# Optimization experiments

Hardware: AMD Instinct MI355X
Metric: run time of the kernel (lower is better)

## Reference

```python
import jax, jax.numpy as jnp
import numpy as np

# --- static config (matches init_kwargs) ---
N = 10000          # nodes
E = 160000         # edges
MULT = 16          # multiplicity (in and out)
NL = 2             # number of irreps (lvals = [0, 1])
DIM = 4            # 1 + 3 spherical dims
EDGE_DIM = 32
HID = 128
RANK = 8           # low-rank radial weight rank
H = 4              # attention heads
HM = MULT // H     # head multiplicity
IDX = np.array([0, 1, 1, 1])  # irrep index for each of the DIM positions


def _radial(ef, w1, bb1, wl, bl, wr, br):
    """Low-rank radial weight: (E, edge_dim) -> (E, NL*MULT, NL*MULT)."""
    h = jax.nn.gelu(ef @ w1 + bb1, approximate=False)
    left = (h @ wl + bl).reshape(-1, NL * MULT, RANK)
    right = (h @ wr + br).reshape(-1, RANK, NL * MULT)
    return left @ right


def _conv(b1, b2, ef, f, src, w1, bb1, wl, bl, wr, br):
    """Equivariant convolution: gather -> basis contract -> radial bmm -> basis."""
    rw = _radial(ef, w1, bb1, wl, bl, wr, br)          # (E, 2*MULT, 2*MULT)
    f_src = f[src]                                      # (E, MULT, DIM)
    t = jnp.einsum('emd,edl->eml', f_src, b1)           # (E, MULT, NL)
    t = t.reshape(E, MULT * NL)                         # row-major, matches torch view
    t = jnp.einsum('erc,ec->er', rw, t)                 # (E, NL*MULT)
    t = t.reshape(E, MULT, NL)                          # (E, out_mult, nl2)
    return jnp.einsum('eml,eld->emd', t, b2)            # (E, MULT, DIM)


def reference(b1, b2, edge_feats, f, src_idx, dst_idx,
              q_w, q_b,
              k_w1, k_b1, k_wl, k_bl, k_wr, k_br,
              v_w1, v_b1, v_wl, v_bl, v_wr, v_br):
    # --- Q: equivariant linear on node features (per-irrep weights) ---
    W = q_w.reshape(NL, MULT, MULT)[IDX]                # (DIM, out_mult, in_mult)
    q = jnp.einsum('dom,nmd->nod', W, f)                # (N, MULT, DIM)
    q = q.at[:, :, 0].add(q_b[:, 0])                    # bias on scalar (l=0) slot

    # --- K, V: equivariant convolutions over edges ---
    k = _conv(b1, b2, edge_feats, f, src_idx, k_w1, k_b1, k_wl, k_bl, k_wr, k_br)
    v = _conv(b1, b2, edge_feats, f, src_idx, v_w1, v_b1, v_wl, v_bl, v_wr, v_br)

    # --- multi-head node_wise attention scores ---
    qh = q.reshape(N, H, HM * DIM)
    kh = k.reshape(E, H, HM * DIM)
    scale = jnp.sqrt(jnp.asarray(HM * DIM, q.dtype))
    scores = jnp.sum(qh[dst_idx] * kh, axis=-1) / scale  # (E, H)

    # --- segment softmax over edges grouped by destination node ---
    m = jax.ops.segment_max(scores, dst_idx, num_segments=N)       # (N, H)
    ex = jnp.exp(scores - m[dst_idx])
    den = jax.ops.segment_sum(ex, dst_idx, num_segments=N)         # (N, H)
    alpha = ex / jnp.maximum(den[dst_idx], 1e-9)                   # (E, H)

    # --- weighted scatter-reduce of values ---
    vh = v.reshape(E, H, HM * DIM)
    out = jax.ops.segment_sum(alpha[..., None] * vh, dst_idx, num_segments=N)
    return out.reshape(N, MULT, DIM)


def setup_inputs() -> dict:
    key = jax.random.key(0)
    ks = jax.random.split(key, 24)
    s = 0.05
    inp = {
        'b1': jax.random.normal(ks[0], (E, DIM, NL), jnp.float32),
        'b2': jax.random.normal(ks[1], (E, NL, DIM), jnp.float32),
        'edge_feats': jax.random.normal(ks[2], (E, EDGE_DIM), jnp.float32),
        'f': jax.random.normal(ks[3], (N, MULT, DIM), jnp.float32),
        'src_idx': jax.random.randint(ks[4], (E,), 0, N),
        'dst_idx': jax.random.randint(ks[5], (E,), 0, N),
        # Q equivariant linear
        'q_w': jax.random.normal(ks[6], (NL * MULT, MULT), jnp.float32) * s,
        'q_b': jnp.zeros((MULT, 1), jnp.float32),
    }
    for i, p in enumerate(['k', 'v']):
        base = 8 + i * 6
        inp[p + '_w1'] = jax.random.normal(ks[base + 0], (EDGE_DIM, HID), jnp.float32) * s
        inp[p + '_b1'] = jnp.zeros((HID,), jnp.float32)
        inp[p + '_wl'] = jax.random.normal(ks[base + 2], (HID, NL * MULT * RANK), jnp.float32) * s
        inp[p + '_bl'] = jnp.zeros((NL * MULT * RANK,), jnp.float32)
        inp[p + '_wr'] = jax.random.normal(ks[base + 4], (HID, RANK * NL * MULT), jnp.float32) * s
        inp[p + '_br'] = jnp.zeros((RANK * NL * MULT,), jnp.float32)
    return inp
```

## Files before the change

kernel.cpp:

```cpp
#include <hip/hip_runtime.h>
#include <hip/hip_bf16.h>
#include <math.h>

#define NNODES 10000
#define NEDGE  160000

typedef unsigned short u16;
using bf16x8 = __attribute__((ext_vector_type(8))) short;
using u16x8  = __attribute__((ext_vector_type(8))) unsigned short;
using f32x4  = __attribute__((ext_vector_type(4))) float;

static __device__ __forceinline__ u16 f2bf(float x) {
  unsigned u = __float_as_uint(x);
  u += 0x7FFFu + ((u >> 16) & 1u);
  return (u16)(u >> 16);
}
static __device__ __forceinline__ float bf2f(u16 h) {
  return __uint_as_float(((unsigned)h) << 16);
}
static __device__ __forceinline__ float fast_gelu(float x) {
  float y = x * __builtin_fmaf(0.07135481283f, x * x, 1.5957691216f);
  float e = __expf(y);
  return x - x * __builtin_amdgcn_rcpf(e + 1.0f);
}

__global__ void __launch_bounds__(256) setup_kernel(
    const float* __restrict__ kwr, const float* __restrict__ kwl,
    const float* __restrict__ vwr, const float* __restrict__ vwl,
    u16* __restrict__ Wsw,
    const float* __restrict__ kw1, const float* __restrict__ vw1,
    u16* __restrict__ W1sw,
    const float* __restrict__ f, const float* __restrict__ qw,
    const float* __restrict__ qb, float* __restrict__ q,
    int* __restrict__ cnt) {
  int b = blockIdx.x, tid = threadIdx.x;
  if (b < 40) {
    int i = b * 256 + tid;
    if (i < NNODES) cnt[i] = 0;
  } else if (b < 552) {
    int idx = (b - 40) * 256 + tid;
    int slot = idx >> 15;
    int w = idx & 32767;
    int j = w & 7, lane = (w >> 3) & 63, ks = (w >> 9) & 3, tg = w >> 11;
    int k   = ks * 32 + ((lane >> 4) << 3) + j;
    int col = (tg << 4) + (lane & 15);
    const float* s = (slot == 0) ? kwr : (slot == 1) ? kwl : (slot == 2) ? vwr : vwl;
    Wsw[idx] = f2bf(s[k * 256 + col]);
  } else if (b < 584) {
    int idx = (b - 552) * 256 + tid;
    int slot = idx >> 12;
    int w = idx & 4095;
    int j = w & 7, lane = (w >> 3) & 63, nt = w >> 9;
    int k   = ((lane >> 4) << 3) + j;
    int col = (nt << 4) + (lane & 15);
    const float* s = (slot == 0) ? kw1 : vw1;
    W1sw[idx] = f2bf(s[k * 128 + col]);
  } else {
    int i = (b - 584) * 256 + tid;
    if (i >= NNODES * 16) return;
    int n = i >> 4, o = i & 15;
    const float* frow = f + (size_t)n * 64;
    float o0 = 0.f, o1 = 0.f, o2 = 0.f, o3 = 0.f;
#pragma unroll
    for (int m = 0; m < 16; ++m) {
      float w0 = qw[o * 16 + m];
      float w1 = qw[(16 + o) * 16 + m];
      o0 += w0 * frow[m * 4 + 0];
      o1 += w1 * frow[m * 4 + 1];
      o2 += w1 * frow[m * 4 + 2];
      o3 += w1 * frow[m * 4 + 3];
    }
    o0 += qb[o];
    float4 r = make_float4(o0, o1, o2, o3);
    *(float4*)(q + (size_t)i * 4) = r;
  }
}

__global__ void csr_count_kernel(const int* __restrict__ dst, int* __restrict__ cnt) {
  int e = blockIdx.x * 256 + threadIdx.x;
  atomicAdd(&cnt[dst[e]], 1);
}
__global__ void __launch_bounds__(1024) csr_scan_kernel(
    const int* __restrict__ cnt, int* __restrict__ rowptr, int* __restrict__ cursor) {
  __shared__ int part[1024];
  int t = threadIdx.x;
  int base = t * 10;
  int s = 0;
#pragma unroll
  for (int i = 0; i < 10; ++i) { int idx = base + i; if (idx < NNODES) s += cnt[idx]; }
  part[t] = s;
  __syncthreads();
  for (int o = 1; o < 1024; o <<= 1) {
    int v = (t >= o) ? part[t - o] : 0;
    __syncthreads();
    part[t] += v;
    __syncthreads();
  }
  int run = (t == 0) ? 0 : part[t - 1];
#pragma unroll
  for (int i = 0; i < 10; ++i) {
    int idx = base + i;
    if (idx < NNODES) { rowptr[idx] = run; cursor[idx] = run; run += cnt[idx]; }
  }
  if (t == 1023) rowptr[NNODES] = run;
}
__global__ void csr_fill_kernel(const int* __restrict__ dst, int* __restrict__ cursor,
                                int* __restrict__ eidx) {
  int e = blockIdx.x * 256 + threadIdx.x;
  int pos = atomicAdd(&cursor[dst[e]], 1);
  eidx[pos] = e;
}

__global__ void t_kernel(const float* __restrict__ f, const float* __restrict__ b1,
                         const int* __restrict__ src, const int* __restrict__ eidx,
                         const float* __restrict__ b2,
                         u16* __restrict__ tbuf, float* __restrict__ b2p) {
  int i = blockIdx.x * 256 + threadIdx.x;
  int re = eidx[i];
  const float* frow = f + (size_t)src[re] * 64;
  const float* be = b1 + (size_t)re * 8;
  float b[8];
#pragma unroll
  for (int k = 0; k < 8; ++k) b[k] = be[k];
  u16* tp = tbuf + (size_t)i * 32;
#pragma unroll
  for (int mh = 0; mh < 4; ++mh) {
    u16x8 ov;
#pragma unroll
    for (int mi = 0; mi < 4; ++mi) {
      int m = mh * 4 + mi;
      float f0 = frow[m * 4 + 0], f1 = frow[m * 4 + 1], f2 = frow[m * 4 + 2], f3 = frow[m * 4 + 3];
#pragma unroll
      for (int l = 0; l < 2; ++l) {
        float t = f0 * b[0 * 2 + l] + f1 * b[1 * 2 + l] + f2 * b[2 * 2 + l] + f3 * b[3 * 2 + l];
        ov[mi * 2 + l] = f2bf(t);
      }
    }
    *(u16x8*)&tp[mh * 8] = ov;
  }
  const float* b2e = b2 + (size_t)re * 8;
  float* bp = b2p + (size_t)i * 8;
  *(float4*)&bp[0] = *(const float4*)&b2e[0];
  *(float4*)&bp[4] = *(const float4*)&b2e[4];
}

__global__ void __launch_bounds__(512) conv_fused_kernel(
    const float* __restrict__ ef, const u16* __restrict__ w1sw,
    const float* __restrict__ b1h,
    const u16* __restrict__ wsw_r, const float* __restrict__ br,
    const u16* __restrict__ wsw_l, const float* __restrict__ bl,
    const u16* __restrict__ tbuf, const float* __restrict__ b2p,
    const int* __restrict__ eidx, u16* __restrict__ kv) {
  __shared__ alignas(16) u16 sA[64 * 136];
  __shared__ alignas(16) u16 t_s[64 * 40];
  __shared__ alignas(16) float b2_s[64 * 12];
  __shared__ alignas(16) float u_s[64 * 12];
  __shared__ alignas(16) float t2_pool[64 * 36];
  float* t2_s = t2_pool;
  u16*   efs  = (u16*)t2_pool;

  int tid = threadIdx.x;
  int wave = tid >> 6, lane = tid & 63, quad = lane >> 4, l16 = lane & 15;
  size_t i0 = (size_t)blockIdx.x * 64;

  if (tid < 256) {
    int row = tid >> 2, seg = tid & 3;
    int pe = eidx[i0 + row];
    const float* ap = ef + (size_t)pe * 32 + seg * 8;
    float4 v0 = *(const float4*)&ap[0];
    float4 v1 = *(const float4*)&ap[4];
    u16x8 ov;
    ov[0] = f2bf(v0.x); ov[1] = f2bf(v0.y); ov[2] = f2bf(v0.z); ov[3] = f2bf(v0.w);
    ov[4] = f2bf(v1.x); ov[5] = f2bf(v1.y); ov[6] = f2bf(v1.z); ov[7] = f2bf(v1.w);
    *(u16x8*)&efs[row * 40 + seg * 8] = ov;
    if (tid < 128) {
      int r2 = tid >> 1, half = tid & 1;
      *(float4*)&b2_s[r2 * 12 + half * 4] = *(const float4*)&b2p[(i0 + r2) * 8 + half * 4];
    }
  } else {
    int j = tid - 256;
    int row = j >> 2, seg = j & 3;
    *(uint4*)&t_s[row * 40 + seg * 8] = *(const uint4*)&tbuf[(i0 + row) * 32 + seg * 8];
  }
  __syncthreads();

  {
    bf16x8 aw = *(const bf16x8*)&w1sw[(size_t)(wave * 64 + lane) * 8];
    float4 bias_h = *(const float4*)&b1h[wave * 16 + quad * 4];
#pragma unroll
    for (int nt = 0; nt < 4; ++nt) {
      bf16x8 be = *(const bf16x8*)&efs[(nt * 16 + l16) * 40 + quad * 8];
      f32x4 acch = __builtin_amdgcn_mfma_f32_16x16x32_bf16(aw, be, (f32x4){0.f, 0.f, 0.f, 0.f}, 0, 0, 0);
      ushort4 hv;
      hv.x = f2bf(fast_gelu(acch[0] + bias_h.x));
      hv.y = f2bf(fast_gelu(acch[1] + bias_h.y));
      hv.z = f2bf(fast_gelu(acch[2] + bias_h.z));
      hv.w = f2bf(fast_gelu(acch[3] + bias_h.w));
      *(ushort4*)&sA[(nt * 16 + l16) * 136 + wave * 16 + quad * 4] = hv;
    }
  }
  __syncthreads();

  f32x4 accr[2][4], accl[2][4];
#pragma unroll
  for (int mtl = 0; mtl < 2; ++mtl)
#pragma unroll
    for (int nt = 0; nt < 4; ++nt) {
      accr[mtl][nt] = (f32x4){0.f, 0.f, 0.f, 0.f};
      accl[mtl][nt] = (f32x4){0.f, 0.f, 0.f, 0.f};
    }
#pragma unroll
  for (int ks = 0; ks < 4; ++ks) {
    bf16x8 bfrag[4];
#pragma unroll
    for (int nt = 0; nt < 4; ++nt)
      bfrag[nt] = *(const bf16x8*)&sA[(nt * 16 + l16) * 136 + ks * 32 + quad * 8];
#pragma unroll
    for (int mtl = 0; mtl < 2; ++mtl) {
      int mtg = wave * 2 + mtl;
      bf16x8 ar = *(const bf16x8*)&wsw_r[(size_t)((mtg * 4 + ks) * 64 + lane) * 8];
      bf16x8 al = *(const bf16x8*)&wsw_l[(size_t)((mtg * 4 + ks) * 64 + lane) * 8];
#pragma unroll
      for (int nt = 0; nt < 4; ++nt) {
        accr[mtl][nt] = __builtin_amdgcn_mfma_f32_16x16x32_bf16(ar, bfrag[nt], accr[mtl][nt], 0, 0, 0);
        accl[mtl][nt] = __builtin_amdgcn_mfma_f32_16x16x32_bf16(al, bfrag[nt], accl[mtl][nt], 0, 0, 0);
      }
    }
  }

  float brv[2][4], blv[2][4];
#pragma unroll
  for (int mtl = 0; mtl < 2; ++mtl)
#pragma unroll
    for (int r = 0; r < 4; ++r) {
      int col = (wave * 2 + mtl) * 16 + quad * 4 + r;
      brv[mtl][r] = br[col];
      blv[mtl][r] = bl[col];
    }

#pragma unroll
  for (int nt = 0; nt < 4; ++nt) {
    int e = nt * 16 + l16;
    ushort4 ta = *(const ushort4*)&t_s[e * 40 + 4 * quad];
    ushort4 tb = *(const ushort4*)&t_s[e * 40 + 16 + 4 * quad];
    float s = (accr[0][nt][0] + brv[0][0]) * bf2f(ta.x)
            + (accr[0][nt][1] + brv[0][1]) * bf2f(ta.y)
            + (accr[0][nt][2] + brv[0][2]) * bf2f(ta.z)
            + (accr[0][nt][3] + brv[0][3]) * bf2f(ta.w)
            + (accr[1][nt][0] + brv[1][0]) * bf2f(tb.x)
            + (accr[1][nt][1] + brv[1][1]) * bf2f(tb.y)
            + (accr[1][nt][2] + brv[1][2]) * bf2f(tb.z)
            + (accr[1][nt][3] + brv[1][3]) * bf2f(tb.w);
    s += __shfl_xor(s, 16);
    s += __shfl_xor(s, 32);
    if (quad == 0) u_s[e * 12 + wave] = s;
  }
  __syncthreads();

#pragma unroll
  for (int nt = 0; nt < 4; ++nt) {
    int e = nt * 16 + l16;
    float4 uv = *(const float4*)&u_s[e * 12 + 4 * (quad & 1)];
#pragma unroll
    for (int mtl = 0; mtl < 2; ++mtl) {
      float s = (accl[mtl][nt][0] + blv[mtl][0]) * uv.x
              + (accl[mtl][nt][1] + blv[mtl][1]) * uv.y
              + (accl[mtl][nt][2] + blv[mtl][2]) * uv.z
              + (accl[mtl][nt][3] + blv[mtl][3]) * uv.w;
      s += __shfl_xor(s, 16);
      if ((quad & 1) == 0)
        t2_s[e * 36 + 4 * wave + 2 * mtl + (quad >> 1)] = s;
    }
  }
  __syncthreads();

  {
    int e = tid >> 3, j = tid & 7;
    float4 t2 = *(const float4*)&t2_s[e * 36 + 4 * j];
    float4 b2a = *(const float4*)&b2_s[e * 12 + 0];
    float4 b2b = *(const float4*)&b2_s[e * 12 + 4];
    u16x8 ov;
    ov[0] = f2bf(t2.x * b2a.x + t2.y * b2b.x);
    ov[1] = f2bf(t2.x * b2a.y + t2.y * b2b.y);
    ov[2] = f2bf(t2.x * b2a.z + t2.y * b2b.z);
    ov[3] = f2bf(t2.x * b2a.w + t2.y * b2b.w);
    ov[4] = f2bf(t2.z * b2a.x + t2.w * b2b.x);
    ov[5] = f2bf(t2.z * b2a.y + t2.w * b2b.y);
    ov[6] = f2bf(t2.z * b2a.z + t2.w * b2b.z);
    ov[7] = f2bf(t2.z * b2a.w + t2.w * b2b.w);
    *(u16x8*)&kv[(i0 + e) * 64 + j * 8] = ov;
  }
}

__global__ void __launch_bounds__(256) attn_gather_kernel(
    const float* __restrict__ q, const u16* __restrict__ kvk,
    const u16* __restrict__ kvv, const int* __restrict__ rowptr,
    float* __restrict__ outp) {
  int tid = threadIdx.x;
  int node = blockIdx.x * 4 + (tid >> 6);
  int lane = tid & 63;
  float qv = q[(size_t)node * 64 + lane];
  int beg = rowptr[node], end = rowptr[node + 1];
  float num = 0.f, den = 0.f;
  for (int idx = beg; idx < end; ++idx) {
    float kf = bf2f(kvk[(size_t)idx * 64 + lane]);
    float p = qv * kf;
    p += __shfl_xor(p, 1, 16);
    p += __shfl_xor(p, 2, 16);
    p += __shfl_xor(p, 4, 16);
    p += __shfl_xor(p, 8, 16);
    float exv = __expf(p * 0.25f);
    den += exv;
    num += exv * bf2f(kvv[(size_t)idx * 64 + lane]);
  }
  outp[(size_t)node * 64 + lane] = num / fmaxf(den, 1e-9f);
}

extern "C" void kernel_launch(void* const* d_in, const int* in_sizes, int n_in,
                              void* d_out, int out_size, void* d_ws, size_t ws_size,
                              hipStream_t stream) {
  const float* b1  = (const float*)d_in[0];
  const float* b2  = (const float*)d_in[1];
  const float* ef  = (const float*)d_in[2];
  const float* f   = (const float*)d_in[3];
  const int*   src = (const int*)d_in[4];
  const int*   dst = (const int*)d_in[5];
  const float* qw  = (const float*)d_in[6];
  const float* qb  = (const float*)d_in[7];
  const float* kw1 = (const float*)d_in[8];
  const float* kb1 = (const float*)d_in[9];
  const float* kwl = (const float*)d_in[10];
  const float* kbl = (const float*)d_in[11];
  const float* kwr = (const float*)d_in[12];
  const float* kbr = (const float*)d_in[13];
  const float* vw1 = (const float*)d_in[14];
  const float* vb1 = (const float*)d_in[15];
  const float* vwl = (const float*)d_in[16];
  const float* vbl = (const float*)d_in[17];
  const float* vwr = (const float*)d_in[18];
  const float* vbr = (const float*)d_in[19];
  float* outp = (float*)d_out;

  char* ws = (char*)d_ws;
  size_t off = 0;
  auto alloc = [&](size_t bytes) {
    char* p = ws + off;
    off += (bytes + 511) & ~(size_t)511;
    return p;
  };
  u16*   Wsw  = (u16*)  alloc((size_t)4 * 32768 * 2);
  u16*   W1sw = (u16*)  alloc((size_t)2 * 4096 * 2);
  u16*   tbuf = (u16*)  alloc((size_t)NEDGE * 32 * 2);
  float* b2p  = (float*)alloc((size_t)NEDGE * 8 * 4);
  u16*   kvk  = (u16*)  alloc((size_t)NEDGE * 64 * 2);
  u16*   kvv  = (u16*)  alloc((size_t)NEDGE * 64 * 2);
  float* qbuf = (float*)alloc((size_t)NNODES * 64 * 4);
  int*   cnt    = (int*)alloc((size_t)NNODES * 4);
  int*   rowptr = (int*)alloc((size_t)(NNODES + 1) * 4);
  int*   cursor = (int*)alloc((size_t)NNODES * 4);
  int*   eidx   = (int*)alloc((size_t)NEDGE * 4);

  setup_kernel<<<1209, 256, 0, stream>>>(kwr, kwl, vwr, vwl, Wsw,
                                         kw1, vw1, W1sw,
                                         f, qw, qb, qbuf, cnt);
  csr_count_kernel<<<625, 256, 0, stream>>>(dst, cnt);
  csr_scan_kernel<<<1, 1024, 0, stream>>>(cnt, rowptr, cursor);
  csr_fill_kernel<<<625, 256, 0, stream>>>(dst, cursor, eidx);

  t_kernel<<<625, 256, 0, stream>>>(f, b1, src, eidx, b2, tbuf, b2p);

  conv_fused_kernel<<<2500, 512, 0, stream>>>(ef, W1sw + 0 * 4096, kb1,
                                              Wsw + 0 * 32768, kbr,
                                              Wsw + 1 * 32768, kbl,
                                              tbuf, b2p, eidx, kvk);
  conv_fused_kernel<<<2500, 512, 0, stream>>>(ef, W1sw + 1 * 4096, vb1,
                                              Wsw + 2 * 32768, vbr,
                                              Wsw + 3 * 32768, vbl,
                                              tbuf, b2p, eidx, kvv);

  attn_gather_kernel<<<2500, 256, 0, stream>>>(qbuf, kvk, kvv, rowptr, outp);
}
```

Measured before the change: 263.6 us.

## Fuse CSR fill with edge prep, pre-permute bf16 edge feats, seed MFMA with bias

Merges the CSR scatter and the per-edge t/b2 preparation into one kernel that writes directly at the sorted position. It also pre-converts edge features to bf16 in sorted order, so the conv kernels read them contiguously without an eidx indirection or an extra barrier. Biases are folded into the MFMA accumulator initial values, and bf16 packing uses paired conversions. The t2 stride changes to 33, and the attention reduction uses DPP instead of shuffles. The cost is an extra bf16 edge-feature buffer and scattered writes in the fill kernel.

```diff
diff --git a/kernel.cpp b/kernel.cpp
--- a/kernel.cpp
+++ b/kernel.cpp
@@ -18,10 +18,21 @@
 static __device__ __forceinline__ float bf2f(u16 h) {
   return __uint_as_float(((unsigned)h) << 16);
 }
+static __device__ __forceinline__ unsigned pack_bf16(float a, float b) {
+  __hip_bfloat162 h = __float22bfloat162_rn(make_float2(a, b));
+  return *(unsigned*)&h;
+}
 static __device__ __forceinline__ float fast_gelu(float x) {
   float y = x * __builtin_fmaf(0.07135481283f, x * x, 1.5957691216f);
   float e = __expf(y);
   return x - x * __builtin_amdgcn_rcpf(e + 1.0f);
+}
+static __device__ __forceinline__ float dpp_red16(float p) {
+  p += __int_as_float(__builtin_amdgcn_update_dpp(0, __float_as_int(p), 0xB1,  0xF, 0xF, true));
+  p += __int_as_float(__builtin_amdgcn_update_dpp(0, __float_as_int(p), 0x4E,  0xF, 0xF, true));
+  p += __int_as_float(__builtin_amdgcn_update_dpp(0, __float_as_int(p), 0x141, 0xF, 0xF, true));
+  p += __int_as_float(__builtin_amdgcn_update_dpp(0, __float_as_int(p), 0x140, 0xF, 0xF, true));
+  return p;
 }
 
 __global__ void __launch_bounds__(256) setup_kernel(
@@ -104,60 +115,61 @@
   }
   if (t == 1023) rowptr[NNODES] = run;
 }
-__global__ void csr_fill_kernel(const int* __restrict__ dst, int* __restrict__ cursor,
-                                int* __restrict__ eidx) {
+
+__global__ void __launch_bounds__(256) fill_t_kernel(
+    const int* __restrict__ dst, const int* __restrict__ src,
+    const float* __restrict__ f, const float* __restrict__ b1,
+    const float* __restrict__ b2, const float* __restrict__ ef,
+    int* __restrict__ cursor,
+    u16* __restrict__ tbuf, float* __restrict__ b2p, u16* __restrict__ efp) {
   int e = blockIdx.x * 256 + threadIdx.x;
   int pos = atomicAdd(&cursor[dst[e]], 1);
-  eidx[pos] = e;
-}
-
-__global__ void t_kernel(const float* __restrict__ f, const float* __restrict__ b1,
-                         const int* __restrict__ src, const int* __restrict__ eidx,
-                         const float* __restrict__ b2,
-                         u16* __restrict__ tbuf, float* __restrict__ b2p) {
-  int i = blockIdx.x * 256 + threadIdx.x;
-  int re = eidx[i];
-  const float* frow = f + (size_t)src[re] * 64;
-  const float* be = b1 + (size_t)re * 8;
+  const float* frow = f + (size_t)src[e] * 64;
+  const float* be = b1 + (size_t)e * 8;
   float b[8];
 #pragma unroll
   for (int k = 0; k < 8; ++k) b[k] = be[k];
-  u16* tp = tbuf + (size_t)i * 32;
+  uint4* tp = (uint4*)(tbuf + (size_t)pos * 32);
 #pragma unroll
   for (int mh = 0; mh < 4; ++mh) {
-    u16x8 ov;
+    unsigned pk[4];
 #pragma unroll
     for (int mi = 0; mi < 4; ++mi) {
       int m = mh * 4 + mi;
       float f0 = frow[m * 4 + 0], f1 = frow[m * 4 + 1], f2 = frow[m * 4 + 2], f3 = frow[m * 4 + 3];
-#pragma unroll
-      for (int l = 0; l < 2; ++l) {
-        float t = f0 * b[0 * 2 + l] + f1 * b[1 * 2 + l] + f2 * b[2 * 2 + l] + f3 * b[3 * 2 + l];
-        ov[mi * 2 + l] = f2bf(t);
-      }
-    }
-    *(u16x8*)&tp[mh * 8] = ov;
-  }
-  const float* b2e = b2 + (size_t)re * 8;
-  float* bp = b2p + (size_t)i * 8;
+      float t0 = f0 * b[0] + f1 * b[2] + f2 * b[4] + f3 * b[6];
+      float t1 = f0 * b[1] + f1 * b[3] + f2 * b[5] + f3 * b[7];
+      pk[mi] = pack_bf16(t0, t1);
+    }
+    tp[mh] = make_uint4(pk[0], pk[1], pk[2], pk[3]);
+  }
+  const float* b2e = b2 + (size_t)e * 8;
+  float* bp = b2p + (size_t)pos * 8;
   *(float4*)&bp[0] = *(const float4*)&b2e[0];
   *(float4*)&bp[4] = *(const float4*)&b2e[4];
+  const float* efe = ef + (size_t)e * 32;
+  uint4* ep = (uint4*)(efp + (size_t)pos * 32);
+#pragma unroll
+  for (int g = 0; g < 4; ++g) {
+    float4 v0 = *(const float4*)&efe[g * 8];
+    float4 v1 = *(const float4*)&efe[g * 8 + 4];
+    ep[g] = make_uint4(pack_bf16(v0.x, v0.y), pack_bf16(v0.z, v0.w),
+                       pack_bf16(v1.x, v1.y), pack_bf16(v1.z, v1.w));
+  }
 }
 
 __global__ void __launch_bounds__(512) conv_fused_kernel(
-    const float* __restrict__ ef, const u16* __restrict__ w1sw,
+    const u16* __restrict__ efp, const u16* __restrict__ w1sw,
     const float* __restrict__ b1h,
     const u16* __restrict__ wsw_r, const float* __restrict__ br,
     const u16* __restrict__ wsw_l, const float* __restrict__ bl,
     const u16* __restrict__ tbuf, const float* __restrict__ b2p,
-    const int* __restrict__ eidx, u16* __restrict__ kv) {
+    u16* __restrict__ kv) {
   __shared__ alignas(16) u16 sA[64 * 136];
   __shared__ alignas(16) u16 t_s[64 * 40];
   __shared__ alignas(16) float b2_s[64 * 12];
   __shared__ alignas(16) float u_s[64 * 12];
-  __shared__ alignas(16) float t2_pool[64 * 36];
-  float* t2_s = t2_pool;
-  u16*   efs  = (u16*)t2_pool;
+  __shared__ alignas(16) float t2_s[64 * 33];
 
   int tid = threadIdx.x;
   int wave = tid >> 6, lane = tid & 63, quad = lane >> 4, l16 = lane & 15;
@@ -165,50 +177,46 @@
 
   if (tid < 256) {
     int row = tid >> 2, seg = tid & 3;
-    int pe = eidx[i0 + row];
-    const float* ap = ef + (size_t)pe * 32 + seg * 8;
-    float4 v0 = *(const float4*)&ap[0];
-    float4 v1 = *(const float4*)&ap[4];
-    u16x8 ov;
-    ov[0] = f2bf(v0.x); ov[1] = f2bf(v0.y); ov[2] = f2bf(v0.z); ov[3] = f2bf(v0.w);
-    ov[4] = f2bf(v1.x); ov[5] = f2bf(v1.y); ov[6] = f2bf(v1.z); ov[7] = f2bf(v1.w);
-    *(u16x8*)&efs[row * 40 + seg * 8] = ov;
-    if (tid < 128) {
-      int r2 = tid >> 1, half = tid & 1;
-      *(float4*)&b2_s[r2 * 12 + half * 4] = *(const float4*)&b2p[(i0 + r2) * 8 + half * 4];
-    }
-  } else {
-    int j = tid - 256;
-    int row = j >> 2, seg = j & 3;
     *(uint4*)&t_s[row * 40 + seg * 8] = *(const uint4*)&tbuf[(i0 + row) * 32 + seg * 8];
-  }
-  __syncthreads();
+  } else if (tid < 384) {
+    int j = tid - 256, row = j >> 1, half = j & 1;
+    *(float4*)&b2_s[row * 12 + half * 4] = *(const float4*)&b2p[(i0 + row) * 8 + half * 4];
+  }
 
   {
     bf16x8 aw = *(const bf16x8*)&w1sw[(size_t)(wave * 64 + lane) * 8];
     float4 bias_h = *(const float4*)&b1h[wave * 16 + quad * 4];
+    f32x4 seed;
+    seed[0] = bias_h.x; seed[1] = bias_h.y; seed[2] = bias_h.z; seed[3] = bias_h.w;
 #pragma unroll
     for (int nt = 0; nt < 4; ++nt) {
-      bf16x8 be = *(const bf16x8*)&efs[(nt * 16 + l16) * 40 + quad * 8];
-      f32x4 acch = __builtin_amdgcn_mfma_f32_16x16x32_bf16(aw, be, (f32x4){0.f, 0.f, 0.f, 0.f}, 0, 0, 0);
-      ushort4 hv;
-      hv.x = f2bf(fast_gelu(acch[0] + bias_h.x));
-      hv.y = f2bf(fast_gelu(acch[1] + bias_h.y));
-      hv.z = f2bf(fast_gelu(acch[2] + bias_h.z));
-      hv.w = f2bf(fast_gelu(acch[3] + bias_h.w));
-      *(ushort4*)&sA[(nt * 16 + l16) * 136 + wave * 16 + quad * 4] = hv;
+      bf16x8 be = *(const bf16x8*)&efp[(i0 + nt * 16 + l16) * 32 + quad * 8];
+      f32x4 acch = __builtin_amdgcn_mfma_f32_16x16x32_bf16(aw, be, seed, 0, 0, 0);
+      unsigned p0 = pack_bf16(fast_gelu(acch[0]), fast_gelu(acch[1]));
+      unsigned p1 = pack_bf16(fast_gelu(acch[2]), fast_gelu(acch[3]));
+      *(uint2*)&sA[(nt * 16 + l16) * 136 + wave * 16 + quad * 4] = make_uint2(p0, p1);
     }
   }
   __syncthreads();
 
+  float4 brv[2], blv[2];
+#pragma unroll
+  for (int mtl = 0; mtl < 2; ++mtl) {
+    int colb = (wave * 2 + mtl) * 16 + quad * 4;
+    brv[mtl] = *(const float4*)&br[colb];
+    blv[mtl] = *(const float4*)&bl[colb];
+  }
   f32x4 accr[2][4], accl[2][4];
 #pragma unroll
   for (int mtl = 0; mtl < 2; ++mtl)
 #pragma unroll
     for (int nt = 0; nt < 4; ++nt) {
-      accr[mtl][nt] = (f32x4){0.f, 0.f, 0.f, 0.f};
-      accl[mtl][nt] = (f32x4){0.f, 0.f, 0.f, 0.f};
-    }
+      accr[mtl][nt][0] = brv[mtl].x; accr[mtl][nt][1] = brv[mtl].y;
+      accr[mtl][nt][2] = brv[mtl].z; accr[mtl][nt][3] = brv[mtl].w;
+      accl[mtl][nt][0] = blv[mtl].x; accl[mtl][nt][1] = blv[mtl].y;
+      accl[mtl][nt][2] = blv[mtl].z; accl[mtl][nt][3] = blv[mtl].w;
+    }
+
 #pragma unroll
   for (int ks = 0; ks < 4; ++ks) {
     bf16x8 bfrag[4];
@@ -228,29 +236,19 @@
     }
   }
 
-  float brv[2][4], blv[2][4];
-#pragma unroll
-  for (int mtl = 0; mtl < 2; ++mtl)
-#pragma unroll
-    for (int r = 0; r < 4; ++r) {
-      int col = (wave * 2 + mtl) * 16 + quad * 4 + r;
-      brv[mtl][r] = br[col];
-      blv[mtl][r] = bl[col];
-    }
-
 #pragma unroll
   for (int nt = 0; nt < 4; ++nt) {
     int e = nt * 16 + l16;
     ushort4 ta = *(const ushort4*)&t_s[e * 40 + 4 * quad];
     ushort4 tb = *(const ushort4*)&t_s[e * 40 + 16 + 4 * quad];
-    float s = (accr[0][nt][0] + brv[0][0]) * bf2f(ta.x)
-            + (accr[0][nt][1] + brv[0][1]) * bf2f(ta.y)
-            + (accr[0][nt][2] + brv[0][2]) * bf2f(ta.z)
-            + (accr[0][nt][3] + brv[0][3]) * bf2f(ta.w)
-            + (accr[1][nt][0] + brv[1][0]) * bf2f(tb.x)
-            + (accr[1][nt][1] + brv[1][1]) * bf2f(tb.y)
-            + (accr[1][nt][2] + brv[1][2]) * bf2f(tb.z)
-            + (accr[1][nt][3] + brv[1][3]) * bf2f(tb.w);
+    float s = accr[0][nt][0] * bf2f(ta.x)
+            + accr[0][nt][1] * bf2f(ta.y)
+            + accr[0][nt][2] * bf2f(ta.z)
+            + accr[0][nt][3] * bf2f(ta.w)
+            + accr[1][nt][0] * bf2f(tb.x)
+            + accr[1][nt][1] * bf2f(tb.y)
+            + accr[1][nt][2] * bf2f(tb.z)
+            + accr[1][nt][3] * bf2f(tb.w);
     s += __shfl_xor(s, 16);
     s += __shfl_xor(s, 32);
     if (quad == 0) u_s[e * 12 + wave] = s;
@@ -263,32 +261,28 @@
     float4 uv = *(const float4*)&u_s[e * 12 + 4 * (quad & 1)];
 #pragma unroll
     for (int mtl = 0; mtl < 2; ++mtl) {
-      float s = (accl[mtl][nt][0] + blv[mtl][0]) * uv.x
-              + (accl[mtl][nt][1] + blv[mtl][1]) * uv.y
-              + (accl[mtl][nt][2] + blv[mtl][2]) * uv.z
-              + (accl[mtl][nt][3] + blv[mtl][3]) * uv.w;
+      float s = accl[mtl][nt][0] * uv.x
+              + accl[mtl][nt][1] * uv.y
+              + accl[mtl][nt][2] * uv.z
+              + accl[mtl][nt][3] * uv.w;
       s += __shfl_xor(s, 16);
       if ((quad & 1) == 0)
-        t2_s[e * 36 + 4 * wave + 2 * mtl + (quad >> 1)] = s;
+        t2_s[e * 33 + 4 * wave + 2 * mtl + (quad >> 1)] = s;
     }
   }
   __syncthreads();
 
   {
     int e = tid >> 3, j = tid & 7;
-    float4 t2 = *(const float4*)&t2_s[e * 36 + 4 * j];
+    const float* tp = &t2_s[e * 33 + 4 * j];
+    float t20 = tp[0], t21 = tp[1], t22 = tp[2], t23 = tp[3];
     float4 b2a = *(const float4*)&b2_s[e * 12 + 0];
     float4 b2b = *(const float4*)&b2_s[e * 12 + 4];
-    u16x8 ov;
-    ov[0] = f2bf(t2.x * b2a.x + t2.y * b2b.x);
-    ov[1] = f2bf(t2.x * b2a.y + t2.y * b2b.y);
-    ov[2] = f2bf(t2.x * b2a.z + t2.y * b2b.z);
-    ov[3] = f2bf(t2.x * b2a.w + t2.y * b2b.w);
-    ov[4] = f2bf(t2.z * b2a.x + t2.w * b2b.x);
-    ov[5] = f2bf(t2.z * b2a.y + t2.w * b2b.y);
-    ov[6] = f2bf(t2.z * b2a.z + t2.w * b2b.z);
-    ov[7] = f2bf(t2.z * b2a.w + t2.w * b2b.w);
-    *(u16x8*)&kv[(i0 + e) * 64 + j * 8] = ov;
+    unsigned q0 = pack_bf16(t20 * b2a.x + t21 * b2b.x, t20 * b2a.y + t21 * b2b.y);
+    unsigned q1 = pack_bf16(t20 * b2a.z + t21 * b2b.z, t20 * b2a.w + t21 * b2b.w);
+    unsigned q2 = pack_bf16(t22 * b2a.x + t23 * b2b.x, t22 * b2a.y + t23 * b2b.y);
+    unsigned q3 = pack_bf16(t22 * b2a.z + t23 * b2b.z, t22 * b2a.w + t23 * b2b.w);
+    *(uint4*)&kv[(i0 + e) * 64 + j * 8] = make_uint4(q0, q1, q2, q3);
   }
 }
 
@@ -304,11 +298,7 @@
   float num = 0.f, den = 0.f;
   for (int idx = beg; idx < end; ++idx) {
     float kf = bf2f(kvk[(size_t)idx * 64 + lane]);
-    float p = qv * kf;
-    p += __shfl_xor(p, 1, 16);
-    p += __shfl_xor(p, 2, 16);
-    p += __shfl_xor(p, 4, 16);
-    p += __shfl_xor(p, 8, 16);
+    float p = dpp_red16(qv * kf);
     float exv = __expf(p * 0.25f);
     den += exv;
     num += exv * bf2f(kvv[(size_t)idx * 64 + lane]);
@@ -352,31 +342,30 @@
   u16*   W1sw = (u16*)  alloc((size_t)2 * 4096 * 2);
   u16*   tbuf = (u16*)  alloc((size_t)NEDGE * 32 * 2);
   float* b2p  = (float*)alloc((size_t)NEDGE * 8 * 4);
+  u16*   efp  = (u16*)  alloc((size_t)NEDGE * 32 * 2);
   u16*   kvk  = (u16*)  alloc((size_t)NEDGE * 64 * 2);
   u16*   kvv  = (u16*)  alloc((size_t)NEDGE * 64 * 2);
   float* qbuf = (float*)alloc((size_t)NNODES * 64 * 4);
   int*   cnt    = (int*)alloc((size_t)NNODES * 4);
   int*   rowptr = (int*)alloc((size_t)(NNODES + 1) * 4);
   int*   cursor = (int*)alloc((size_t)NNODES * 4);
-  int*   eidx   = (int*)alloc((size_t)NEDGE * 4);
 
   setup_kernel<<<1209, 256, 0, stream>>>(kwr, kwl, vwr, vwl, Wsw,
                                          kw1, vw1, W1sw,
                                          f, qw, qb, qbuf, cnt);
   csr_count_kernel<<<625, 256, 0, stream>>>(dst, cnt);
   csr_scan_kernel<<<1, 1024, 0, stream>>>(cnt, rowptr, cursor);
-  csr_fill_kernel<<<625, 256, 0, stream>>>(dst, cursor, eidx);
-
-  t_kernel<<<625, 256, 0, stream>>>(f, b1, src, eidx, b2, tbuf, b2p);
-
-  conv_fused_kernel<<<2500, 512, 0, stream>>>(ef, W1sw + 0 * 4096, kb1,
+  fill_t_kernel<<<625, 256, 0, stream>>>(dst, src, f, b1, b2, ef,
+                                         cursor, tbuf, b2p, efp);
+
+  conv_fused_kernel<<<2500, 512, 0, stream>>>(efp, W1sw + 0 * 4096, kb1,
                                               Wsw + 0 * 32768, kbr,
                                               Wsw + 1 * 32768, kbl,
-                                              tbuf, b2p, eidx, kvk);
-  conv_fused_kernel<<<2500, 512, 0, stream>>>(ef, W1sw + 1 * 4096, vb1,
+                                              tbuf, b2p, kvk);
+  conv_fused_kernel<<<2500, 512, 0, stream>>>(efp, W1sw + 1 * 4096, vb1,
                                               Wsw + 2 * 32768, vbr,
                                               Wsw + 3 * 32768, vbl,
-                                              tbuf, b2p, eidx, kvv);
+                                              tbuf, b2p, kvv);
 
   attn_gather_kernel<<<2500, 256, 0, stream>>>(qbuf, kvk, kvv, rowptr, outp);
 }
```

New measurement: 290.3 us. 10.1% more time.
